# Optimization experiments

Measured on AMD Instinct MI355X. Metric: run time of the kernel, lower is better.

## Reference

```python
import jax, jax.numpy as jnp
import numpy as np
import math

D_MODEL = 1024
N_HEADS = 16
HEAD_DIM = D_MODEL // N_HEADS  # 64
B, T = 2, 2048


def _rotate_half(x):
    x1, x2 = jnp.split(x, 2, axis=-1)
    return jnp.concatenate([-x2, x1], axis=-1)


def _rope_sin_cos(seq_len, dim, dtype=jnp.float32):
    # matches RotaryEmbedding: inv_freq over even indices, emb = [freqs, freqs]
    inv_freq = 1.0 / (10000.0 ** (jnp.arange(0, dim, 2, dtype=dtype) / dim))
    t = jnp.arange(seq_len, dtype=dtype)
    freqs = jnp.einsum('i,j->ij', t, inv_freq)          # [T, dim/2]
    emb = jnp.concatenate((freqs, freqs), axis=-1)      # [T, dim]
    sin = jnp.sin(emb)[None, :, None, :]                # [1, T, 1, dim]
    cos = jnp.cos(emb)[None, :, None, :]
    return sin, cos


def setup_inputs() -> dict:
    key = jax.random.key(0)
    k1, k2, k3 = jax.random.split(key, 3)
    x = jax.random.normal(k1, (B, T, D_MODEL), dtype=jnp.float32)
    # causal mask broadcast over batch and heads: [1, 1, T, T]
    mask = jnp.tril(jnp.ones((T, T), dtype=bool))[None, None]
    w_qkv = jax.random.normal(k2, (D_MODEL, 3 * D_MODEL), dtype=jnp.float32) / math.sqrt(D_MODEL)
    w_out = jax.random.normal(k3, (D_MODEL, D_MODEL), dtype=jnp.float32) / math.sqrt(D_MODEL)
    return {"x": x, "mask": mask, "w_qkv": w_qkv, "w_out": w_out}


def reference(x, mask, w_qkv, w_out):
    Bx, Tx, Dx = x.shape
    qkv = x @ w_qkv                                     # [B, T, 3D]
    q, k, v = jnp.split(qkv, 3, axis=-1)
    q = q.reshape(Bx, Tx, N_HEADS, HEAD_DIM)
    k = k.reshape(Bx, Tx, N_HEADS, HEAD_DIM)
    v = v.reshape(Bx, Tx, N_HEADS, HEAD_DIM)
    sin, cos = _rope_sin_cos(Tx, HEAD_DIM, x.dtype)
    q = q * cos + _rotate_half(q) * sin
    k = k * cos + _rotate_half(k) * sin
    scores = jnp.einsum('bthd,bThd->bhtT', q, k) / math.sqrt(HEAD_DIM)
    scores = jnp.where(mask, scores, -1e10)
    probs = jax.nn.softmax(scores, axis=-1)             # [B, H, T, T]
    out = jnp.einsum('bhtT,bThd->bthd', probs, v)
    out = out.reshape(Bx, Tx, Dx)
    return out @ w_out
```

## Files before the change

### kernel.cpp

```cpp
#include <hip/hip_runtime.h>
#include <math.h>

typedef unsigned short u16;
typedef __attribute__((ext_vector_type(8))) short short8;
typedef __attribute__((ext_vector_type(4))) float f32x4;
typedef __attribute__((ext_vector_type(16))) float f32x16;
typedef __attribute__((ext_vector_type(4))) unsigned uint4v;

__device__ __forceinline__ u16 f2bf(float f) {
  unsigned int u = __float_as_uint(f);
  u += 0x7fffu + ((u >> 16) & 1u);
  return (u16)(u >> 16);
}
__device__ __forceinline__ float bf2f(u16 h) {
  return __uint_as_float(((unsigned int)h) << 16);
}

__device__ __forceinline__ f32x4 mfma16(short8 a, short8 b, f32x4 c) {
  return __builtin_amdgcn_mfma_f32_16x16x32_bf16(a, b, c, 0, 0, 0);
}
__device__ __forceinline__ f32x16 mfma32(short8 a, short8 b, f32x16 c) {
  return __builtin_amdgcn_mfma_f32_32x32x16_bf16(a, b, c, 0, 0, 0);
}

__device__ __forceinline__ unsigned cvtpk_bf16(float lo, float hi) {
  unsigned r;
  asm("v_cvt_pk_bf16_f32 %0, %1, %2" : "=v"(r) : "v"(lo), "v"(hi));
  return r;
}

__device__ __forceinline__ void xchg32(unsigned x, unsigned y, int hi,
                                       unsigned& a, unsigned& b) {
  unsigned xs = (unsigned)__shfl_xor((int)x, 32);
  unsigned ys = (unsigned)__shfl_xor((int)y, 32);
  a = hi ? ys : x;
  b = hi ? y : xs;
}

#define NEG_BIG (-1e30f)

__device__ __forceinline__ void glds16(const u16* g, u16* l) {
  __builtin_amdgcn_global_load_lds(
      (const __attribute__((address_space(1))) unsigned int*)g,
      (__attribute__((address_space(3))) unsigned int*)l, 16, 0, 0);
}

__global__ __launch_bounds__(256) void detect_dtype3(const u16* __restrict__ a,
                                                     const u16* __restrict__ bb,
                                                     const u16* __restrict__ c,
                                                     int* __restrict__ flags) {
  const u16* x = (blockIdx.x == 0) ? a : (blockIdx.x == 1) ? bb : c;
  __shared__ int cnt;
  if (threadIdx.x == 0) cnt = 0;
  __syncthreads();
  int my = 0;
  for (int i = threadIdx.x; i < 4096; i += 256) {
    float v = bf2f(x[2 * i]);
    float av = fabsf(v);
    if (v == 0.0f || (av >= 1e-4f && av <= 100.0f)) my++;
  }
  atomicAdd(&cnt, my);
  __syncthreads();
  if (threadIdx.x == 0) flags[blockIdx.x] = (cnt > 2458) ? 1 : 0;
}

__global__ __launch_bounds__(256) void prep_all(const void* __restrict__ wqkv,
                                                const void* __restrict__ wout,
                                                const void* __restrict__ xin,
                                                u16* __restrict__ wqkvT,
                                                u16* __restrict__ woutT,
                                                u16* __restrict__ xb,
                                                float2* __restrict__ tab,
                                                const int* __restrict__ flags) {
  int z = blockIdx.z;
  int tid = threadIdx.x;
  if (z == 2) {
    if (blockIdx.x >= 16 || blockIdx.y >= 16) return;
    int idx = (blockIdx.y * 16 + blockIdx.x) * 256 + tid;
    int t = idx >> 5, d = idx & 31;
    float invf = expf(-(float)d * 0.28782313662425575f);
    float s, c;
    sincosf((float)t * invf, &s, &c);
    tab[idx] = make_float2(c, s);
    return;
  }
  if (z == 3) {
    bool isbf = (flags[0] != 0);
    int tg = (blockIdx.y * 48 + blockIdx.x) * 256 + tid;
    for (int i = tg; i < 524288; i += 196608) {
      int base = i * 8;
      if (isbf) {
        *(short8*)(xb + base) = *(const short8*)((const u16*)xin + base);
      } else {
        const float* xf = (const float*)xin;
        f32x4 x0 = *(const f32x4*)(xf + base);
        f32x4 x1 = *(const f32x4*)(xf + base + 4);
        short8 o;
#pragma unroll
        for (int u = 0; u < 4; ++u) { o[u] = (short)f2bf(x0[u]); o[u + 4] = (short)f2bf(x1[u]); }
        *(short8*)(xb + base) = o;
      }
    }
    return;
  }
  const void* in = (z == 0) ? wqkv : wout;
  u16* out = (z == 0) ? wqkvT : woutT;
  int C = (z == 0) ? 3072 : 1024;
  const int R = 1024;
  bool isbf = (flags[z + 1] != 0);
  if (z == 1 && blockIdx.x >= 16) return;
  __shared__ float tile[64][68];
  int tc = blockIdx.x * 64, tr = blockIdx.y * 64;
  int r = tid >> 3, cg = (tid & 7) << 3;
#pragma unroll
  for (int p = 0; p < 2; ++p) {
    int row = r + p * 32;
    if (isbf) {
      short8 v = *(const short8*)((const u16*)in + (size_t)(tr + row) * C + tc + cg);
#pragma unroll
      for (int u = 0; u < 8; ++u) tile[row][cg + u] = bf2f((u16)v[u]);
    } else {
      const float* inf = (const float*)in + (size_t)(tr + row) * C + tc + cg;
#pragma unroll
      for (int u = 0; u < 8; ++u) tile[row][cg + u] = inf[u];
    }
  }
  __syncthreads();
#pragma unroll
  for (int p = 0; p < 2; ++p) {
    int orow = r + p * 32;
    short8 v;
#pragma unroll
    for (int u = 0; u < 8; ++u) v[u] = (short)f2bf(tile[cg + u][orow]);
    *(short8*)(out + (size_t)(tc + orow) * R + tr + cg) = v;
  }
}

__device__ __forceinline__ void qkv_epilogue3(f32x4 acc[4][4], int bm, int bn,
                                              int wm, int wn, int quad, int lane15,
                                              int lane, const float2* __restrict__ tab,
                                              u16* Qo, u16* Ko, u16* VTo, u16* myE) {
  int nbase = bn + wn * 64;
  int h = (nbase & 1023) >> 6;
  if (nbase < 2048) {
    int l8 = lane15 & 7, lh = lane15 >> 3;
#pragma unroll
    for (int i = 0; i < 4; ++i) {
#pragma unroll
      for (int r = 0; r < 4; ++r) {
        int mloc = i * 16 + quad * 4 + r;
        int t = (bm + wm * 64 + mloc) & 2047;
        float2 cs0 = tab[t * 32 + lane15];
        float2 cs1 = tab[t * 32 + 16 + lane15];
        float v0 = acc[i][0][r], v1 = acc[i][1][r], v2 = acc[i][2][r], v3 = acc[i][3][r];
        int m7 = mloc & 7;
        u16* rowp = myE + mloc * 64 + l8;
        rowp[((0 + lh) ^ m7) * 8] = f2bf(v0 * cs0.x - v2 * cs0.y);
        rowp[((2 + lh) ^ m7) * 8] = f2bf(v1 * cs1.x - v3 * cs1.y);
        rowp[((4 + lh) ^ m7) * 8] = f2bf(v2 * cs0.x + v0 * cs0.y);
        rowp[((6 + lh) ^ m7) * 8] = f2bf(v3 * cs1.x + v1 * cs1.y);
      }
    }
    asm volatile("s_waitcnt lgkmcnt(0)" ::: "memory");
    u16* dst = (nbase < 1024) ? Qo : Ko;
#pragma unroll
    for (int p = 0; p < 8; ++p) {
      int f = p * 64 + lane;
      int mr = f >> 3, nc = f & 7;
      short8 val = *(const short8*)(myE + mr * 64 + (nc ^ (mr & 7)) * 8);
      int g = bm + wm * 64 + mr;
      int bI = g >> 11, tI = g & 2047;
      *(short8*)(dst + ((size_t)(bI * 16 + h) * 2048 + tI) * 64 + nc * 8) = val;
    }
  } else {
#pragma unroll
    for (int i = 0; i < 4; ++i)
#pragma unroll
      for (int j = 0; j < 4; ++j)
#pragma unroll
        for (int r = 0; r < 4; ++r) {
          int col = i * 16 + quad * 4 + r;
          int slot = (col >> 3) ^ (lane15 & 7);
          myE[(j * 16 + lane15) * 64 + slot * 8 + (col & 7)] = f2bf(acc[i][j][r]);
        }
    asm volatile("s_waitcnt lgkmcnt(0)" ::: "memory");
    int g0 = bm + wm * 64;
    int bI = g0 >> 11, t0 = g0 & 2047;
#pragma unroll
    for (int p = 0; p < 8; ++p) {
      int f = p * 64 + lane;
      int dr = f >> 3, tc = f & 7;
      short8 val = *(const short8*)(myE + dr * 64 + (tc ^ (dr & 7)) * 8);
      *(short8*)(VTo + ((size_t)(bI * 16 + h) * 64 + dr) * 2048 + t0 + tc * 8) = val;
    }
  }
}

__device__ __forceinline__ void stage256(const u16* __restrict__ X,
                                         const u16* __restrict__ WT,
                                         u16* lAq, u16* lBq,
                                         int bm, int bn, int k0, int tid) {
  const int K = 1024;
#pragma unroll
  for (int p = 0; p < 4; ++p) {
    int cid = p * 512 + tid;
    int r = cid >> 3;
    int cs = (cid & 7) ^ (r & 7);
    int dst = (cid & ~63) * 8;
    glds16(X + (size_t)(bm + r) * K + k0 + cs * 8, lAq + dst);
    glds16(WT + (size_t)(bn + r) * K + k0 + cs * 8, lBq + dst);
  }
}

__device__ __forceinline__ void qkv_step(const u16* lAq, const u16* lBq,
                                         f32x4 acc[8][4], int wm, int wn,
                                         int lane15, int quad) {
  short8 bfr[2][4];
#pragma unroll
  for (int j = 0; j < 4; ++j) {
    int row = wn * 64 + j * 16 + lane15;
    int ro = row * 64, r7 = row & 7;
    bfr[0][j] = *(const short8*)(lBq + ro + (quad ^ r7) * 8);
    bfr[1][j] = *(const short8*)(lBq + ro + ((4 + quad) ^ r7) * 8);
  }
#pragma unroll
  for (int qd = 0; qd < 4; ++qd) {
    short8 afr[2][2];
#pragma unroll
    for (int i2 = 0; i2 < 2; ++i2) {
      int row = wm * 128 + (qd * 2 + i2) * 16 + lane15;
      int ro = row * 64, r7 = row & 7;
      afr[i2][0] = *(const short8*)(lAq + ro + (quad ^ r7) * 8);
      afr[i2][1] = *(const short8*)(lAq + ro + ((4 + quad) ^ r7) * 8);
    }
    __builtin_amdgcn_s_setprio(1);
#pragma unroll
    for (int ks = 0; ks < 2; ++ks)
#pragma unroll
      for (int i2 = 0; i2 < 2; ++i2)
#pragma unroll
        for (int j = 0; j < 4; ++j)
          acc[qd * 2 + i2][j] = mfma16(afr[i2][ks], bfr[ks][j], acc[qd * 2 + i2][j]);
    __builtin_amdgcn_s_setprio(0);
  }
}

__global__ __launch_bounds__(512, 2) void gemm_qkv_256(const u16* __restrict__ X,
                                                       const u16* __restrict__ WT,
                                                       const float2* __restrict__ tab,
                                                       u16* __restrict__ Qo,
                                                       u16* __restrict__ Ko,
                                                       u16* __restrict__ VTo) {
  __shared__ u16 sh[65536];
  int tid = threadIdx.x;
  int wave = tid >> 6, lane = tid & 63;
  int lane15 = lane & 15, quad = lane >> 4;
  int wm = wave >> 2, wn = wave & 3;
  int swz = (blockIdx.x & 7) * 24 + (blockIdx.x >> 3);
  int bm = (swz / 12) * 256, bn = (swz % 12) * 256;
  f32x4 acc[8][4] = {};

  stage256(X, WT, sh, sh + 32768, bm, bn, 0, tid);

#pragma unroll 1
  for (int kt = 0; kt < 15; ++kt) {
    int q = kt & 1;
    stage256(X, WT, sh + (q ^ 1) * 16384, sh + 32768 + (q ^ 1) * 16384,
             bm, bn, (kt + 1) * 64, tid);
    asm volatile("s_waitcnt vmcnt(8)" ::: "memory");
    __builtin_amdgcn_sched_barrier(0);
    asm volatile("s_barrier" ::: "memory");
    qkv_step(sh + q * 16384, sh + 32768 + q * 16384, acc, wm, wn, lane15, quad);
    asm volatile("s_barrier" ::: "memory");
  }
  asm volatile("s_waitcnt vmcnt(0)" ::: "memory");
  __builtin_amdgcn_sched_barrier(0);
  asm volatile("s_barrier" ::: "memory");
  qkv_step(sh + 16384, sh + 32768 + 16384, acc, wm, wn, lane15, quad);
  __syncthreads();

  u16* myE = sh + wave * 8192;
  int nbase = bn + wn * 64;
  int h = (nbase & 1023) >> 6;
  if (nbase < 2048) {
    int l8 = lane15 & 7, lh = lane15 >> 3;
#pragma unroll
    for (int i = 0; i < 8; ++i) {
#pragma unroll
      for (int r = 0; r < 4; ++r) {
        int mloc = i * 16 + quad * 4 + r;
        int t = (bm + wm * 128 + mloc) & 2047;
        float2 cs0 = tab[t * 32 + lane15];
        float2 cs1 = tab[t * 32 + 16 + lane15];
        float v0 = acc[i][0][r], v1 = acc[i][1][r], v2 = acc[i][2][r], v3 = acc[i][3][r];
        int m7 = mloc & 7;
        u16* rowp = myE + mloc * 64 + l8;
        rowp[((0 + lh) ^ m7) * 8] = f2bf(v0 * cs0.x - v2 * cs0.y);
        rowp[((2 + lh) ^ m7) * 8] = f2bf(v1 * cs1.x - v3 * cs1.y);
        rowp[((4 + lh) ^ m7) * 8] = f2bf(v2 * cs0.x + v0 * cs0.y);
        rowp[((6 + lh) ^ m7) * 8] = f2bf(v3 * cs1.x + v1 * cs1.y);
      }
    }
    asm volatile("s_waitcnt lgkmcnt(0)" ::: "memory");
    u16* dst = (nbase < 1024) ? Qo : Ko;
#pragma unroll
    for (int p = 0; p < 16; ++p) {
      int f = p * 64 + lane;
      int mr = f >> 3, nc = f & 7;
      short8 val = *(const short8*)(myE + mr * 64 + (nc ^ (mr & 7)) * 8);
      int g = bm + wm * 128 + mr;
      int bI = g >> 11, tI = g & 2047;
      *(short8*)(dst + ((size_t)(bI * 16 + h) * 2048 + tI) * 64 + nc * 8) = val;
    }
  } else {
#pragma unroll
    for (int i = 0; i < 8; ++i)
#pragma unroll
      for (int j = 0; j < 4; ++j)
#pragma unroll
        for (int r = 0; r < 4; ++r) {
          int col = i * 16 + quad * 4 + r;
          int slot = (col >> 3) ^ (lane15 & 7);
          myE[(j * 16 + lane15) * 128 + slot * 8 + (col & 7)] = f2bf(acc[i][j][r]);
        }
    asm volatile("s_waitcnt lgkmcnt(0)" ::: "memory");
    int g0 = bm + wm * 128;
    int bI = g0 >> 11, t0 = g0 & 2047;
#pragma unroll
    for (int p = 0; p < 16; ++p) {
      int f = p * 64 + lane;
      int dr = f >> 4, tc = f & 15;
      short8 val = *(const short8*)(myE + dr * 128 + (tc ^ (dr & 7)) * 8);
      *(short8*)(VTo + ((size_t)(bI * 16 + h) * 64 + dr) * 2048 + t0 + tc * 8) = val;
    }
  }
}

__global__ __launch_bounds__(256) void gemm_qkv_rope(const void* __restrict__ Xv,
                                                     const u16* __restrict__ WT,
                                                     const float2* __restrict__ tab,
                                                     u16* __restrict__ Qo,
                                                     u16* __restrict__ Ko,
                                                     u16* __restrict__ VTo,
                                                     const int* __restrict__ flag) {
  const int K = 1024;
  __shared__ u16 buf[16384];
  u16* lA = buf;
  u16* lB = buf + 5120;
  bool isbf = (*flag != 0);
  int tid = threadIdx.x;
  int wave = tid >> 6, lane = tid & 63;
  int lane15 = lane & 15, quad = lane >> 4;
  int wm = wave >> 1, wn = wave & 1;
  int bm = blockIdx.x * 128, bn = blockIdx.y * 128;
  int sr = tid >> 2, scg = (tid & 3) << 3;
  f32x4 acc[4][4] = {};
  for (int k0 = 0; k0 < K; k0 += 32) {
    __syncthreads();
#pragma unroll
    for (int p = 0; p < 2; ++p) {
      int row = sr + p * 64;
      if (isbf) {
        *(short8*)(lA + row * 40 + scg) =
            *(const short8*)((const u16*)Xv + (size_t)(bm + row) * K + k0 + scg);
      } else {
        const float* xf = (const float*)Xv + (size_t)(bm + row) * K + k0 + scg;
        f32x4 x0 = *(const f32x4*)(xf);
        f32x4 x1 = *(const f32x4*)(xf + 4);
        short8 o;
#pragma unroll
        for (int u = 0; u < 4; ++u) { o[u] = (short)f2bf(x0[u]); o[u + 4] = (short)f2bf(x1[u]); }
        *(short8*)(lA + row * 40 + scg) = o;
      }
      *(short8*)(lB + row * 40 + scg) = *(const short8*)(WT + (size_t)(bn + row) * K + k0 + scg);
    }
    __syncthreads();
    short8 af[4], bf[4];
#pragma unroll
    for (int i = 0; i < 4; ++i)
      af[i] = *(const short8*)(lA + (wm * 64 + i * 16 + lane15) * 40 + quad * 8);
#pragma unroll
    for (int j = 0; j < 4; ++j)
      bf[j] = *(const short8*)(lB + (wn * 64 + j * 16 + lane15) * 40 + quad * 8);
#pragma unroll
    for (int i = 0; i < 4; ++i)
#pragma unroll
      for (int j = 0; j < 4; ++j)
        acc[i][j] = mfma16(af[i], bf[j], acc[i][j]);
  }
  __syncthreads();
  qkv_epilogue3(acc, bm, bn, wm, wn, quad, lane15, lane, tab, Qo, Ko, VTo,
                buf + wave * 4096);
}

__device__ __forceinline__ short8 lds_frag(const u16* buf, int row, int chunk) {
  int s = chunk ^ (row & 7);
  return *(const short8*)(buf + row * 64 + s * 8);
}

__device__ __forceinline__ void stage_tile(const u16* gK, const u16* gV,
                                           u16* lK, u16* lV, int wave, int lane) {
#pragma unroll
  for (int p = 0; p < 2; ++p) {
    int f = (p * 4 + wave) * 64 + lane;
    int r = f >> 3;
    int c = (f & 7) ^ (r & 7);
    glds16(gK + (size_t)r * 64 + c * 8, lK + (p * 4 + wave) * 512);
    glds16(gV + (size_t)r * 2048 + c * 8, lV + (p * 4 + wave) * 512);
  }
}

__global__ __launch_bounds__(256, 2) void attn_fused(const u16* __restrict__ Q,
                                                     const u16* __restrict__ K,
                                                     const u16* __restrict__ VT,
                                                     u16* __restrict__ Ao) {
  int bx = blockIdx.x;
  int bh = bx & 31;
  int a = bx >> 5;
  int g = (a & 1) ? (15 - (a >> 1)) : (a >> 1);
  int b = bh >> 4, h = bh & 15;
  int tid = threadIdx.x, wave = tid >> 6, lane = tid & 63;
  int l31 = lane & 31, hi = lane >> 5;
  int q0w = g * 128 + wave * 32;
  const u16* Qb = Q + (size_t)bh * 2048 * 64;
  const u16* Kb = K + (size_t)bh * 2048 * 64;
  const u16* Vb = VT + (size_t)bh * 64 * 2048;

  __shared__ u16 Kl[2][64 * 64];
  __shared__ u16 Vl[2][64 * 64];

  short8 qb[4];
#pragma unroll
  for (int c = 0; c < 4; ++c)
    qb[c] = *(const short8*)(Qb + (size_t)(q0w + l31) * 64 + c * 16 + hi * 8);

  f32x16 Od0 = {}, Od1 = {};
  float ts[4] = {0.f, 0.f, 0.f, 0.f};

  int ntiles = 2 * g + 2;
  stage_tile(Kb, Vb, Kl[0], Vl[0], wave, lane);

#pragma unroll 1
  for (int kt = 0; kt < ntiles; ++kt) {
    int kbase = kt * 64;
    int cur = kt & 1;
    __syncthreads();
    if (kt + 1 < ntiles)
      stage_tile(Kb + (size_t)(kbase + 64) * 64, Vb + kbase + 64,
                 Kl[cur ^ 1], Vl[cur ^ 1], wave, lane);

    if (kbase <= q0w + 31) {
      bool diag = (kbase + 63 > q0w);
#pragma unroll
      for (int s = 0; s < 2; ++s) {
        f32x16 st = {};
#pragma unroll
        for (int c = 0; c < 4; ++c) {
          short8 ka = lds_frag(Kl[cur], s * 32 + l31, c * 2 + hi);
          st = mfma32(ka, qb[c], st);
        }
        float p[16];
#pragma unroll
        for (int reg = 0; reg < 16; ++reg) {
          int klocal = (reg & 3) + 8 * (reg >> 2) + 4 * hi;
          float pv = __expf(fmaf(st[reg], 0.125f, -8.0f));
          if (diag && (kbase + s * 32 + klocal > q0w + l31)) pv = 0.f;
          p[reg] = pv;
          ts[reg & 3] += pv;
        }
        unsigned w01 = cvtpk_bf16(p[0], p[1]);
        unsigned w23 = cvtpk_bf16(p[2], p[3]);
        unsigned w45 = cvtpk_bf16(p[4], p[5]);
        unsigned w67 = cvtpk_bf16(p[6], p[7]);
        unsigned w89 = cvtpk_bf16(p[8], p[9]);
        unsigned wab = cvtpk_bf16(p[10], p[11]);
        unsigned wcd = cvtpk_bf16(p[12], p[13]);
        unsigned wef = cvtpk_bf16(p[14], p[15]);
        unsigned a0, a1, a2, a3, c0, c1, c2, c3;
        xchg32(w01, w45, hi, a0, a2);
        xchg32(w23, w67, hi, a1, a3);
        xchg32(w89, wcd, hi, c0, c2);
        xchg32(wab, wef, hi, c1, c3);
        union UU { uint4v u; short8 s8; };
        UU u0; u0.u = (uint4v){a0, a1, a2, a3};
        UU u1; u1.u = (uint4v){c0, c1, c2, c3};
        short8 pa[2] = {u0.s8, u1.s8};
#pragma unroll
        for (int t = 0; t < 2; ++t) {
          int kchunk = s * 4 + t * 2 + hi;
          short8 vb0 = lds_frag(Vl[cur], l31, kchunk);
          Od0 = mfma32(pa[t], vb0, Od0);
          short8 vb1 = lds_frag(Vl[cur], 32 + l31, kchunk);
          Od1 = mfma32(pa[t], vb1, Od1);
        }
      }
    }
  }
  float tsum = (ts[0] + ts[1]) + (ts[2] + ts[3]);
  float fsum = tsum + __shfl_xor(tsum, 32);
  float rl = 1.f / fsum;
#pragma unroll
  for (int reg = 0; reg < 16; ++reg) {
    int qp = (reg & 3) + 8 * (reg >> 2) + 4 * hi;
    float r = __shfl(rl, qp);
    int t = q0w + qp;
    size_t rowo = (size_t)(b * 2048 + t) * 1024 + h * 64;
    Ao[rowo + l31] = f2bf(Od0[reg] * r);
    Ao[rowo + 32 + l31] = f2bf(Od1[reg] * r);
  }
}

__global__ __launch_bounds__(256) void gemm_out(const u16* __restrict__ A,
                                                const u16* __restrict__ WT,
                                                float* __restrict__ out) {
  const int K = 1024;
  __shared__ u16 lA[64 * 128];
  __shared__ u16 lB[128 * 128];
  int tid = threadIdx.x;
  int wave = tid >> 6, lane = tid & 63;
  int lane15 = lane & 15, quad = lane >> 4;
  int wm = wave >> 1, wn = wave & 1;
  int bm = blockIdx.x * 64, bn = blockIdx.y * 128;
  f32x4 acc[2][4] = {};
  for (int k0 = 0; k0 < K; k0 += 128) {
    __syncthreads();
#pragma unroll
    for (int p = 0; p < 4; ++p) {
      int g = p * 4 + wave;
      int f = g * 64 + lane;
      int r = f >> 4;
      int c16 = (f & 15) ^ (r & 15);
      glds16(A + (size_t)(bm + r) * K + k0 + c16 * 8, lA + g * 512);
    }
#pragma unroll
    for (int p = 0; p < 8; ++p) {
      int g = p * 4 + wave;
      int f = g * 64 + lane;
      int r = f >> 4;
      int c16 = (f & 15) ^ (r & 15);
      glds16(WT + (size_t)(bn + r) * K + k0 + c16 * 8, lB + g * 512);
    }
    __syncthreads();
#pragma unroll
    for (int ks = 0; ks < 4; ++ks) {
      int so = ((ks * 4 + quad) ^ lane15) * 8;
      short8 af[2], bf[4];
#pragma unroll
      for (int i = 0; i < 2; ++i)
        af[i] = *(const short8*)(lA + (wm * 32 + i * 16 + lane15) * 128 + so);
#pragma unroll
      for (int j = 0; j < 4; ++j)
        bf[j] = *(const short8*)(lB + (wn * 64 + j * 16 + lane15) * 128 + so);
#pragma unroll
      for (int i = 0; i < 2; ++i)
#pragma unroll
        for (int j = 0; j < 4; ++j)
          acc[i][j] = mfma16(af[i], bf[j], acc[i][j]);
    }
  }
#pragma unroll
  for (int i = 0; i < 2; ++i)
#pragma unroll
    for (int r = 0; r < 4; ++r) {
      int m = bm + wm * 32 + i * 16 + quad * 4 + r;
      size_t rowo = (size_t)m * 1024 + bn + wn * 64 + lane15;
      out[rowo] = acc[i][0][r];
      out[rowo + 16] = acc[i][1][r];
      out[rowo + 32] = acc[i][2][r];
      out[rowo + 48] = acc[i][3][r];
    }
}

__global__ void ws_sentinel(float* out, float val) {
  if (threadIdx.x == 0) out[1] = val;
}

extern "C" void kernel_launch(void* const* d_in, const int* in_sizes, int n_in,
                              void* d_out, int out_size, void* d_ws, size_t ws_size,
                              hipStream_t stream) {
  (void)out_size;
  const void* x = nullptr;
  const void* w_qkv = nullptr;
  const void* w_out = nullptr;
  for (int i = 0; i < n_in; ++i) {
    if (in_sizes[i] == 4194304 && !x) x = d_in[i];
    else if (in_sizes[i] == 3145728 && !w_qkv) w_qkv = d_in[i];
    else if (in_sizes[i] == 1048576 && !w_out) w_out = d_in[i];
  }
  float* out = (float*)d_out;

  const size_t EL_B = 32 + 4194304 + 1048576 + 3 * 4194304 + 262144;
  const size_t REQ_B = EL_B * 2;
  const size_t REQ_A = (EL_B + 4194304) * 2;
  if (ws_size < REQ_B) {
    ws_sentinel<<<1, 64, 0, stream>>>(out, 1.0e6f + 1000.0f * (float)(ws_size >> 20));
    return;
  }
  int* flags = (int*)d_ws;
  u16* base = (u16*)d_ws + 32;
  u16* wqkvT = base;
  u16* attnw = base;
  u16* woutT = base + 4194304;
  u16* Qw = woutT + 1048576;
  u16* Kw = Qw + 4194304;
  u16* VTw = Kw + 4194304;
  float2* tab = (float2*)(VTw + 4194304);
  u16* xb = VTw + 4194304 + 262144;

  detect_dtype3<<<3, 256, 0, stream>>>((const u16*)x, (const u16*)w_qkv,
                                       (const u16*)w_out, flags);
  if (ws_size >= REQ_A) {
    prep_all<<<dim3(48, 16, 4), 256, 0, stream>>>(w_qkv, w_out, x, wqkvT, woutT,
                                                  xb, tab, flags);
    gemm_qkv_256<<<dim3(192), dim3(512), 0, stream>>>(xb, wqkvT, tab, Qw, Kw, VTw);
  } else {
    prep_all<<<dim3(48, 16, 3), 256, 0, stream>>>(w_qkv, w_out, x, wqkvT, woutT,
                                                  nullptr, tab, flags);
    gemm_qkv_rope<<<dim3(32, 24), 256, 0, stream>>>(x, wqkvT, tab, Qw, Kw, VTw, flags + 0);
  }
  attn_fused<<<512, 256, 0, stream>>>(Qw, Kw, VTw, attnw);
  gemm_out<<<dim3(64, 8), 256, 0, stream>>>(attnw, woutT, out);
}
```

Before: 214.7 us.

## Shrink attention blocks to 64 queries and use permlane32 swaps

The attention kernel now uses 128-thread blocks, each covering 64 query rows, with 1024 blocks instead of 512. Tile order is snake-balanced within groups of eight. Causal skipping moves to 32-key sub-tiles, which skips more masked work. The shfl_xor-based half-wave exchanges of the packed P fragments and the row sum are replaced with v_permlane32_swap, cutting cross-lane traffic. Smaller blocks mean each K/V tile staged into LDS is reused by fewer waves, so global and LDS traffic per query goes up.

Result: no change. 212.8 us (-0.9%).

```diff
diff --git a/kernel.cpp b/kernel.cpp
--- a/kernel.cpp
+++ b/kernel.cpp
@@ -6,6 +6,7 @@
 typedef __attribute__((ext_vector_type(4))) float f32x4;
 typedef __attribute__((ext_vector_type(16))) float f32x16;
 typedef __attribute__((ext_vector_type(4))) unsigned uint4v;
+typedef __attribute__((ext_vector_type(2))) unsigned uint2v;
 
 __device__ __forceinline__ u16 f2bf(float f) {
   unsigned int u = __float_as_uint(f);
@@ -29,12 +30,10 @@
   return r;
 }
 
-__device__ __forceinline__ void xchg32(unsigned x, unsigned y, int hi,
-                                       unsigned& a, unsigned& b) {
-  unsigned xs = (unsigned)__shfl_xor((int)x, 32);
-  unsigned ys = (unsigned)__shfl_xor((int)y, 32);
-  a = hi ? ys : x;
-  b = hi ? y : xs;
+__device__ __forceinline__ void xchg32p(unsigned& x, unsigned& y) {
+  uint2v r = __builtin_amdgcn_permlane32_swap(x, y, false, false);
+  x = r[0];
+  y = r[1];
 }
 
 #define NEG_BIG (-1e30f)
@@ -398,30 +397,32 @@
   return *(const short8*)(buf + row * 64 + s * 8);
 }
 
-__device__ __forceinline__ void stage_tile(const u16* gK, const u16* gV,
-                                           u16* lK, u16* lV, int wave, int lane) {
-#pragma unroll
-  for (int p = 0; p < 2; ++p) {
-    int f = (p * 4 + wave) * 64 + lane;
-    int r = f >> 3;
-    int c = (f & 7) ^ (r & 7);
-    glds16(gK + (size_t)r * 64 + c * 8, lK + (p * 4 + wave) * 512);
-    glds16(gV + (size_t)r * 2048 + c * 8, lV + (p * 4 + wave) * 512);
-  }
-}
-
-__global__ __launch_bounds__(256, 2) void attn_fused(const u16* __restrict__ Q,
-                                                     const u16* __restrict__ K,
-                                                     const u16* __restrict__ VT,
-                                                     u16* __restrict__ Ao) {
+__device__ __forceinline__ void stage_tile2(const u16* gK, const u16* gV,
+                                            u16* lK, u16* lV, int tid) {
+#pragma unroll
+  for (int p = 0; p < 4; ++p) {
+    int cid = p * 128 + tid;
+    int r = cid >> 3;
+    int c = (cid & 7) ^ (r & 7);
+    int dst = (cid & ~63) * 8;
+    glds16(gK + (size_t)r * 64 + c * 8, lK + dst);
+    glds16(gV + (size_t)r * 2048 + c * 8, lV + dst);
+  }
+}
+
+__global__ __launch_bounds__(128) void attn_fused(const u16* __restrict__ Q,
+                                                  const u16* __restrict__ K,
+                                                  const u16* __restrict__ VT,
+                                                  u16* __restrict__ Ao) {
   int bx = blockIdx.x;
   int bh = bx & 31;
-  int a = bx >> 5;
-  int g = (a & 1) ? (15 - (a >> 1)) : (a >> 1);
+  int tp = bx >> 5;
+  int aq = tp >> 3, bq = tp & 7;
+  int tau = aq * 8 + ((aq & 1) ? (7 - bq) : bq);
   int b = bh >> 4, h = bh & 15;
   int tid = threadIdx.x, wave = tid >> 6, lane = tid & 63;
   int l31 = lane & 31, hi = lane >> 5;
-  int q0w = g * 128 + wave * 32;
+  int q0w = tau * 64 + wave * 32;
   const u16* Qb = Q + (size_t)bh * 2048 * 64;
   const u16* Kb = K + (size_t)bh * 2048 * 64;
   const u16* Vb = VT + (size_t)bh * 64 * 2048;
@@ -437,8 +438,8 @@
   f32x16 Od0 = {}, Od1 = {};
   float ts[4] = {0.f, 0.f, 0.f, 0.f};
 
-  int ntiles = 2 * g + 2;
-  stage_tile(Kb, Vb, Kl[0], Vl[0], wave, lane);
+  int ntiles = tau + 1;
+  stage_tile2(Kb, Vb, Kl[0], Vl[0], tid);
 
 #pragma unroll 1
   for (int kt = 0; kt < ntiles; ++kt) {
@@ -446,58 +447,59 @@
     int cur = kt & 1;
     __syncthreads();
     if (kt + 1 < ntiles)
-      stage_tile(Kb + (size_t)(kbase + 64) * 64, Vb + kbase + 64,
-                 Kl[cur ^ 1], Vl[cur ^ 1], wave, lane);
-
-    if (kbase <= q0w + 31) {
-      bool diag = (kbase + 63 > q0w);
-#pragma unroll
-      for (int s = 0; s < 2; ++s) {
-        f32x16 st = {};
-#pragma unroll
-        for (int c = 0; c < 4; ++c) {
-          short8 ka = lds_frag(Kl[cur], s * 32 + l31, c * 2 + hi);
-          st = mfma32(ka, qb[c], st);
-        }
-        float p[16];
-#pragma unroll
-        for (int reg = 0; reg < 16; ++reg) {
-          int klocal = (reg & 3) + 8 * (reg >> 2) + 4 * hi;
-          float pv = __expf(fmaf(st[reg], 0.125f, -8.0f));
-          if (diag && (kbase + s * 32 + klocal > q0w + l31)) pv = 0.f;
-          p[reg] = pv;
-          ts[reg & 3] += pv;
-        }
-        unsigned w01 = cvtpk_bf16(p[0], p[1]);
-        unsigned w23 = cvtpk_bf16(p[2], p[3]);
-        unsigned w45 = cvtpk_bf16(p[4], p[5]);
-        unsigned w67 = cvtpk_bf16(p[6], p[7]);
-        unsigned w89 = cvtpk_bf16(p[8], p[9]);
-        unsigned wab = cvtpk_bf16(p[10], p[11]);
-        unsigned wcd = cvtpk_bf16(p[12], p[13]);
-        unsigned wef = cvtpk_bf16(p[14], p[15]);
-        unsigned a0, a1, a2, a3, c0, c1, c2, c3;
-        xchg32(w01, w45, hi, a0, a2);
-        xchg32(w23, w67, hi, a1, a3);
-        xchg32(w89, wcd, hi, c0, c2);
-        xchg32(wab, wef, hi, c1, c3);
-        union UU { uint4v u; short8 s8; };
-        UU u0; u0.u = (uint4v){a0, a1, a2, a3};
-        UU u1; u1.u = (uint4v){c0, c1, c2, c3};
-        short8 pa[2] = {u0.s8, u1.s8};
-#pragma unroll
-        for (int t = 0; t < 2; ++t) {
-          int kchunk = s * 4 + t * 2 + hi;
-          short8 vb0 = lds_frag(Vl[cur], l31, kchunk);
-          Od0 = mfma32(pa[t], vb0, Od0);
-          short8 vb1 = lds_frag(Vl[cur], 32 + l31, kchunk);
-          Od1 = mfma32(pa[t], vb1, Od1);
-        }
+      stage_tile2(Kb + (size_t)(kbase + 64) * 64, Vb + kbase + 64,
+                  Kl[cur ^ 1], Vl[cur ^ 1], tid);
+
+#pragma unroll
+    for (int s = 0; s < 2; ++s) {
+      int lo = kbase + s * 32;
+      if (lo > q0w + 31) continue;
+      bool diag = (lo + 31 > q0w);
+      f32x16 st = {};
+#pragma unroll
+      for (int c = 0; c < 4; ++c) {
+        short8 ka = lds_frag(Kl[cur], s * 32 + l31, c * 2 + hi);
+        st = mfma32(ka, qb[c], st);
       }
+      float p[16];
+#pragma unroll
+      for (int reg = 0; reg < 16; ++reg) {
+        int klocal = (reg & 3) + 8 * (reg >> 2) + 4 * hi;
+        float pv = __expf(fmaf(st[reg], 0.125f, -8.0f));
+        if (diag && (lo + klocal > q0w + l31)) pv = 0.f;
+        p[reg] = pv;
+        ts[reg & 3] += pv;
+      }
+      unsigned w01 = cvtpk_bf16(p[0], p[1]);
+      unsigned w23 = cvtpk_bf16(p[2], p[3]);
+      unsigned w45 = cvtpk_bf16(p[4], p[5]);
+      unsigned w67 = cvtpk_bf16(p[6], p[7]);
+      unsigned w89 = cvtpk_bf16(p[8], p[9]);
+      unsigned wab = cvtpk_bf16(p[10], p[11]);
+      unsigned wcd = cvtpk_bf16(p[12], p[13]);
+      unsigned wef = cvtpk_bf16(p[14], p[15]);
+      xchg32p(w01, w45);
+      xchg32p(w23, w67);
+      xchg32p(w89, wcd);
+      xchg32p(wab, wef);
+      union UU { uint4v u; short8 s8; };
+      UU u0; u0.u = (uint4v){w01, w23, w45, w67};
+      UU u1; u1.u = (uint4v){w89, wab, wcd, wef};
+      short8 pa[2] = {u0.s8, u1.s8};
+#pragma unroll
+      for (int t = 0; t < 2; ++t) {
+        int kchunk = s * 4 + t * 2 + hi;
+        short8 vb0 = lds_frag(Vl[cur], l31, kchunk);
+        Od0 = mfma32(pa[t], vb0, Od0);
+        short8 vb1 = lds_frag(Vl[cur], 32 + l31, kchunk);
+        Od1 = mfma32(pa[t], vb1, Od1);
+      }
     }
   }
   float tsum = (ts[0] + ts[1]) + (ts[2] + ts[3]);
-  float fsum = tsum + __shfl_xor(tsum, 32);
+  unsigned tl = __float_as_uint(tsum), th = tl;
+  xchg32p(tl, th);
+  float fsum = __uint_as_float(tl) + __uint_as_float(th);
   float rl = 1.f / fsum;
 #pragma unroll
   for (int reg = 0; reg < 16; ++reg) {
@@ -618,6 +620,6 @@
                                                   nullptr, tab, flags);
     gemm_qkv_rope<<<dim3(32, 24), 256, 0, stream>>>(x, wqkvT, tab, Qw, Kw, VTw, flags + 0);
   }
-  attn_fused<<<512, 256, 0, stream>>>(Qw, Kw, VTw, attnw);
+  attn_fused<<<1024, 128, 0, stream>>>(Qw, Kw, VTw, attnw);
   gemm_out<<<dim3(64, 8), 256, 0, stream>>>(attnw, woutT, out);
 }
```
